# Kernel optimization log

Hardware: AMD Instinct MI355X
Metric: run time of the kernel (lower is better)

## Reference

```python
import jax, jax.numpy as jnp
import numpy as np

EPS = 1e-6  # F.pairwise_distance default eps, added elementwise to the diff


def _locality(feat_map):
    # feat_map: [T, D, H, W]
    T, D, H, W = feat_map.shape
    f = feat_map
    f2 = f * f

    # Per-row (H) and per-column (W) partial sums of v and v^2.
    s1_h = jnp.sum(f, axis=(1, 3))   # [T, H]
    s2_h = jnp.sum(f2, axis=(1, 3))  # [T, H]
    s1_w = jnp.sum(f, axis=(1, 2))   # [T, W]
    s2_w = jnp.sum(f2, axis=(1, 2))  # [T, W]

    # pairwise_distance(x, 0, p=2, eps) = sqrt(sum((x + eps)^2))
    #                                   = sqrt(sum x^2 + 2*eps*sum x + eps^2 * n)
    def ga_suffix(s1, s2, n_per):
        # group i = slice [i:]  -> suffix cumulative sums
        L = s1.shape[1]
        suf1 = jnp.cumsum(s1[:, ::-1], axis=1)[:, ::-1]
        suf2 = jnp.cumsum(s2[:, ::-1], axis=1)[:, ::-1]
        n = n_per * (L - jnp.arange(L, dtype=s1.dtype))  # elements in suffix slice
        return jnp.sqrt(suf2 + 2.0 * EPS * suf1 + (EPS * EPS) * n)

    def ga_prefix(s1, s2, n_per):
        # group j = slice [:j+1] -> prefix cumulative sums
        L = s1.shape[1]
        pre1 = jnp.cumsum(s1, axis=1)
        pre2 = jnp.cumsum(s2, axis=1)
        n = n_per * (jnp.arange(L, dtype=s1.dtype) + 1.0)
        return jnp.sqrt(pre2 + 2.0 * EPS * pre1 + (EPS * EPS) * n)

    ga1 = ga_suffix(s1_h, s2_h, float(D * W))  # [T, H]
    ga2 = ga_prefix(s1_h, s2_h, float(D * W))  # [T, H]
    ga3 = ga_suffix(s1_w, s2_w, float(D * H))  # [T, W]
    ga4 = ga_prefix(s1_w, s2_w, float(D * H))  # [T, W]

    # pairwise_distance(ga, 0, p=1, eps) = sum |ga + eps| ; ga >= 0 so = sum(ga) + eps*L
    def l1_mean(ga):
        return jnp.mean(jnp.sum(ga + EPS, axis=1))

    tot = (l1_mean(ga1) + l1_mean(ga2) + l1_mean(ga3) + l1_mean(ga4)) / 4.0
    log10 = lambda x: jnp.log(x) / jnp.log(jnp.asarray(10.0, x.dtype))
    return tot, log10(ga1), log10(ga2), log10(ga3), log10(ga4)


def setup_inputs() -> dict:
    key = jax.random.key(0)
    feat_map = jax.random.normal(key, (32, 256, 56, 56), dtype=jnp.float32)
    return {"feat_map": feat_map}


def reference(feat_map):
    return _locality(feat_map)
```

## Files before the change

### kernel.cpp

```cpp
#include <hip/hip_runtime.h>
#include <math.h>

#define EPS 1e-6f


__global__ __launch_bounds__(832) void loc_reduce(const float* __restrict__ f,
                                                  float* __restrict__ ws) {
    const int t   = blockIdx.x >> 3;
    const int dg  = blockIdx.x & 7;
    const int tid = threadIdx.x;

    __shared__ float ls[224];
    for (int k = tid; k < 224; k += 832) ls[k] = 0.f;
    __syncthreads();

    if (tid < 784) {
        const int h = tid / 14;
        const int v = tid % 14;
        const float4* p4 = reinterpret_cast<const float4*>(
            f + (size_t)t * 802816 + (size_t)(dg * 32) * 3136) + (size_t)h * 14 + v;

        float s10 = 0.f, s11 = 0.f, s12 = 0.f, s13 = 0.f;
        float s20 = 0.f, s21 = 0.f, s22 = 0.f, s23 = 0.f;
        #pragma unroll 4
        for (int d = 0; d < 32; ++d) {
            float4 x = p4[(size_t)d * 784];
            s10 += x.x; s11 += x.y; s12 += x.z; s13 += x.w;
            s20 += x.x * x.x; s21 += x.y * x.y; s22 += x.z * x.z; s23 += x.w * x.w;
        }

        atomicAdd(&ls[0 * 56 + h], s10 + s11 + s12 + s13);
        atomicAdd(&ls[1 * 56 + h], s20 + s21 + s22 + s23);
        atomicAdd(&ls[2 * 56 + 4 * v + 0], s10);
        atomicAdd(&ls[2 * 56 + 4 * v + 1], s11);
        atomicAdd(&ls[2 * 56 + 4 * v + 2], s12);
        atomicAdd(&ls[2 * 56 + 4 * v + 3], s13);
        atomicAdd(&ls[3 * 56 + 4 * v + 0], s20);
        atomicAdd(&ls[3 * 56 + 4 * v + 1], s21);
        atomicAdd(&ls[3 * 56 + 4 * v + 2], s22);
        atomicAdd(&ls[3 * 56 + 4 * v + 3], s23);
    }
    __syncthreads();

    if (tid < 224) ws[(size_t)blockIdx.x * 224 + tid] = ls[tid];
}

__global__ __launch_bounds__(1024) void loc_finalize(const float* __restrict__ ws,
                                                     float* __restrict__ out) {
    __shared__ float sums[7168];
    const int tid = threadIdx.x;

    #pragma unroll
    for (int k = 0; k < 7; ++k) {
        const int o = tid + 1024 * k;
        const int t = o / 224;
        const int r = o % 224;
        float a = 0.f;
        #pragma unroll
        for (int dg = 0; dg < 8; ++dg) a += ws[(size_t)(t * 8 + dg) * 224 + r];
        sums[o] = a;
    }
    __syncthreads();

    if (tid < 64) {
        const int t    = tid & 31;
        const bool isW = tid >= 32;

        const float* s1 = &sums[(t * 4 + (isW ? 2 : 0)) * 56];
        const float* s2 = &sums[(t * 4 + (isW ? 3 : 1)) * 56];
        float* osuf = out + 1 + (isW ? 3584 : 0)    + t * 56;
        float* opre = out + 1 + (isW ? 5376 : 1792) + t * 56;

        const float n_per = 14336.f;
        float part = 0.f;

        float a1 = 0.f, a2 = 0.f;
        for (int i = 55; i >= 0; --i) {
            a1 += s1[i]; a2 += s2[i];
            const float n  = n_per * (float)(56 - i);
            const float ga = sqrtf(a2 + 2.0f * EPS * a1 + (EPS * EPS) * n);
            osuf[i] = log10f(ga);
            part += ga + EPS;
        }
        a1 = 0.f; a2 = 0.f;
        for (int i = 0; i < 56; ++i) {
            a1 += s1[i]; a2 += s2[i];
            const float n  = n_per * (float)(i + 1);
            const float ga = sqrtf(a2 + 2.0f * EPS * a1 + (EPS * EPS) * n);
            opre[i] = log10f(ga);
            part += ga + EPS;
        }

        #pragma unroll
        for (int off = 32; off; off >>= 1) part += __shfl_down(part, off);
        if (tid == 0) out[0] = part * (1.0f / 128.0f);
    }
}

extern "C" void kernel_launch(void* const* d_in, const int* in_sizes, int n_in,
                              void* d_out, int out_size, void* d_ws, size_t ws_size,
                              hipStream_t stream) {
    const float* f = (const float*)d_in[0];
    float* out = (float*)d_out;
    float* ws  = (float*)d_ws;

    loc_reduce<<<dim3(256), dim3(832), 0, stream>>>(f, ws);
    loc_finalize<<<dim3(1), dim3(1024), 0, stream>>>(ws, out);
}
```

Baseline: 48.15 us.

## Repartition reduction into flat 256-thread blocks over spatial-channel chunks

The reduce kernel moves from 256 blocks of 832 threads (one block per batch and 32-channel group) to 1568 blocks of 256 threads. Each thread sums 16 channels spaced 16 apart at one flattened float4 position, so memory access is contiguous across the whole block and there are more blocks to fill the GPU's compute units. In exchange the single-block finalize kernel must sum 49 partials per output instead of 8, which lengthens that serial tail and makes the workspace larger.

Result: slower. 68.07 us (+41.4%).

```diff
diff --git a/kernel.cpp b/kernel.cpp
--- a/kernel.cpp
+++ b/kernel.cpp
@@ -4,45 +4,45 @@
 #define EPS 1e-6f
 
 
-__global__ __launch_bounds__(832) void loc_reduce(const float* __restrict__ f,
+__global__ __launch_bounds__(256) void loc_reduce(const float* __restrict__ f,
                                                   float* __restrict__ ws) {
-    const int t   = blockIdx.x >> 3;
-    const int dg  = blockIdx.x & 7;
+    const int b   = blockIdx.x;
+    const int t   = b / 49;
+    const int pb  = b % 49;
     const int tid = threadIdx.x;
+    const int r   = pb * 256 + tid;
+    const int pos = r % 784;
+    const int h   = pos / 14;
+    const int v   = pos % 14;
+
+    const float4* p = reinterpret_cast<const float4*>(f) + (size_t)t * 200704 + r;
+
+    float s10 = 0.f, s11 = 0.f, s12 = 0.f, s13 = 0.f;
+    float s20 = 0.f, s21 = 0.f, s22 = 0.f, s23 = 0.f;
+
+    for (int i = 0; i < 16; ++i) {
+        float4 x = p[(size_t)i * 12544];
+        s10 += x.x; s11 += x.y; s12 += x.z; s13 += x.w;
+        s20 += x.x * x.x; s21 += x.y * x.y; s22 += x.z * x.z; s23 += x.w * x.w;
+    }
 
     __shared__ float ls[224];
-    for (int k = tid; k < 224; k += 832) ls[k] = 0.f;
+    if (tid < 224) ls[tid] = 0.f;
     __syncthreads();
 
-    if (tid < 784) {
-        const int h = tid / 14;
-        const int v = tid % 14;
-        const float4* p4 = reinterpret_cast<const float4*>(
-            f + (size_t)t * 802816 + (size_t)(dg * 32) * 3136) + (size_t)h * 14 + v;
-
-        float s10 = 0.f, s11 = 0.f, s12 = 0.f, s13 = 0.f;
-        float s20 = 0.f, s21 = 0.f, s22 = 0.f, s23 = 0.f;
-        #pragma unroll 4
-        for (int d = 0; d < 32; ++d) {
-            float4 x = p4[(size_t)d * 784];
-            s10 += x.x; s11 += x.y; s12 += x.z; s13 += x.w;
-            s20 += x.x * x.x; s21 += x.y * x.y; s22 += x.z * x.z; s23 += x.w * x.w;
-        }
-
-        atomicAdd(&ls[0 * 56 + h], s10 + s11 + s12 + s13);
-        atomicAdd(&ls[1 * 56 + h], s20 + s21 + s22 + s23);
-        atomicAdd(&ls[2 * 56 + 4 * v + 0], s10);
-        atomicAdd(&ls[2 * 56 + 4 * v + 1], s11);
-        atomicAdd(&ls[2 * 56 + 4 * v + 2], s12);
-        atomicAdd(&ls[2 * 56 + 4 * v + 3], s13);
-        atomicAdd(&ls[3 * 56 + 4 * v + 0], s20);
-        atomicAdd(&ls[3 * 56 + 4 * v + 1], s21);
-        atomicAdd(&ls[3 * 56 + 4 * v + 2], s22);
-        atomicAdd(&ls[3 * 56 + 4 * v + 3], s23);
-    }
+    atomicAdd(&ls[0 * 56 + h], s10 + s11 + s12 + s13);
+    atomicAdd(&ls[1 * 56 + h], s20 + s21 + s22 + s23);
+    atomicAdd(&ls[112 + 4 * v + 0], s10);
+    atomicAdd(&ls[112 + 4 * v + 1], s11);
+    atomicAdd(&ls[112 + 4 * v + 2], s12);
+    atomicAdd(&ls[112 + 4 * v + 3], s13);
+    atomicAdd(&ls[168 + 4 * v + 0], s20);
+    atomicAdd(&ls[168 + 4 * v + 1], s21);
+    atomicAdd(&ls[168 + 4 * v + 2], s22);
+    atomicAdd(&ls[168 + 4 * v + 3], s23);
     __syncthreads();
 
-    if (tid < 224) ws[(size_t)blockIdx.x * 224 + tid] = ls[tid];
+    if (tid < 224) ws[(size_t)b * 224 + tid] = ls[tid];
 }
 
 __global__ __launch_bounds__(1024) void loc_finalize(const float* __restrict__ ws,
@@ -52,12 +52,12 @@
 
     #pragma unroll
     for (int k = 0; k < 7; ++k) {
-        const int o = tid + 1024 * k;
-        const int t = o / 224;
-        const int r = o % 224;
+        const int o  = tid + 1024 * k;
+        const int t  = o / 224;
+        const int k2 = o % 224;
         float a = 0.f;
-        #pragma unroll
-        for (int dg = 0; dg < 8; ++dg) a += ws[(size_t)(t * 8 + dg) * 224 + r];
+        for (int pb = 0; pb < 49; ++pb)
+            a += ws[(size_t)(t * 49 + pb) * 224 + k2];
         sums[o] = a;
     }
     __syncthreads();
@@ -66,8 +66,8 @@
         const int t    = tid & 31;
         const bool isW = tid >= 32;
 
-        const float* s1 = &sums[(t * 4 + (isW ? 2 : 0)) * 56];
-        const float* s2 = &sums[(t * 4 + (isW ? 3 : 1)) * 56];
+        const float* s1 = &sums[t * 224 + (isW ? 112 : 0)];
+        const float* s2 = &sums[t * 224 + (isW ? 168 : 56)];
         float* osuf = out + 1 + (isW ? 3584 : 0)    + t * 56;
         float* opre = out + 1 + (isW ? 5376 : 1792) + t * 56;
 
@@ -104,6 +104,6 @@
     float* out = (float*)d_out;
     float* ws  = (float*)d_ws;
 
-    loc_reduce<<<dim3(256), dim3(832), 0, stream>>>(f, ws);
+    loc_reduce<<<dim3(1568), dim3(256), 0, stream>>>(f, ws);
     loc_finalize<<<dim3(1), dim3(1024), 0, stream>>>(ws, out);
 }
```
